# Kernel optimization log

Hardware: AMD Instinct MI355X
Metric: run time of the kernel (lower is better)

Reference implementation:

```python
import jax, jax.numpy as jnp
import numpy as np

S, B, IN, OUT = 32, 256, 1024, 1024

def setup_inputs() -> dict:
    key = jax.random.key(0)
    ks = jax.random.split(key, 7)
    return {
        "input": jax.random.normal(ks[0], (S, B, IN), dtype=jnp.float32),
        "weight_mu": jax.random.normal(ks[1], (OUT, IN), dtype=jnp.float32) * 0.1,
        "weight_rho": jax.random.normal(ks[2], (OUT, IN), dtype=jnp.float32) - 3.0,
        "bias_mu": jax.random.normal(ks[3], (OUT,), dtype=jnp.float32) * 0.1,
        "bias_rho": jax.random.normal(ks[4], (OUT,), dtype=jnp.float32) - 3.0,
        "eps_w": jax.random.normal(ks[5], (S, OUT, IN), dtype=jnp.float32),
        "eps_b": jax.random.normal(ks[6], (S, OUT), dtype=jnp.float32),
    }

def reference(input, weight_mu, weight_rho, bias_mu, bias_rho, eps_w, eps_b):
    # sigma = log(1 + exp(rho))  (softplus)
    weight_sigma = jax.nn.softplus(weight_rho)              # (out, in)
    bias_sigma = jax.nn.softplus(bias_rho)                  # (out,)
    # reparameterized samples: (S, out, in) and (S, out)
    weight = weight_mu[None, :, :] + weight_sigma[None, :, :] * eps_w
    bias = bias_mu[None, :] + bias_sigma[None, :] * eps_b
    # batch_linear: per-sample x @ W^T + b
    out = jnp.einsum('sbi,soi->sbo', input, weight) + bias[:, None, :]
    return out
```

## Files before the change

kernel.cpp:

```cpp
#include <hip/hip_runtime.h>
#include <hip/hip_bf16.h>

constexpr int kS   = 32;
constexpr int kB   = 256;
constexpr int kIN  = 1024;
constexpr int kOUT = 1024;
constexpr int BN   = 64;
constexpr int BK   = 32;
constexpr int CK   = 256;

typedef __bf16 v4bf __attribute__((ext_vector_type(4)));
typedef __bf16 v8bf __attribute__((ext_vector_type(8)));
typedef float  v4f  __attribute__((ext_vector_type(4)));

__device__ __forceinline__ float softplus_f(float x) {
    return fmaxf(x, 0.0f) + log1pf(expf(-fabsf(x)));
}
__device__ __forceinline__ unsigned int bfbits(float x) {
    __bf16 h = (__bf16)x;
    unsigned short u;
    __builtin_memcpy(&u, &h, 2);
    return (unsigned int)u;
}
__device__ __forceinline__ float asf(unsigned int u) {
    float f; __builtin_memcpy(&f, &u, 4); return f;
}

__global__ void sigma_pack(const float* __restrict__ mu, const float* __restrict__ rho,
                           uint4* __restrict__ ms) {
    int gid = blockIdx.x * blockDim.x + threadIdx.x;
    float4 m = reinterpret_cast<const float4*>(mu)[gid];
    float4 r = reinterpret_cast<const float4*>(rho)[gid];
    uint4 o;
    o.x = bfbits(m.x) | (bfbits(softplus_f(r.x)) << 16);
    o.y = bfbits(m.y) | (bfbits(softplus_f(r.y)) << 16);
    o.z = bfbits(m.z) | (bfbits(softplus_f(r.z)) << 16);
    o.w = bfbits(m.w) | (bfbits(softplus_f(r.w)) << 16);
    ms[gid] = o;
}

__global__ void xcast_kernel(const float* __restrict__ X, __bf16* __restrict__ Xb) {
    size_t i = ((size_t)blockIdx.x * blockDim.x + threadIdx.x) * 8;
    float4 a = *reinterpret_cast<const float4*>(X + i);
    float4 b = *reinterpret_cast<const float4*>(X + i + 4);
    v8bf r;
    r[0] = (__bf16)a.x; r[1] = (__bf16)a.y; r[2] = (__bf16)a.z; r[3] = (__bf16)a.w;
    r[4] = (__bf16)b.x; r[5] = (__bf16)b.y; r[6] = (__bf16)b.z; r[7] = (__bf16)b.w;
    *reinterpret_cast<v8bf*>(Xb + i) = r;
}

#define GLDS16(g, l) __builtin_amdgcn_global_load_lds(                      \
    (const __attribute__((address_space(1))) void*)(g),                     \
    (__attribute__((address_space(3))) void*)(l), 16, 0, 0)

template<bool XBF>
__global__ __launch_bounds__(256) void dv_main(
        const void* __restrict__ Xv,
        const unsigned int* __restrict__ MS,
        const float* __restrict__ Ew,
        const float* __restrict__ Bmu,
        const float* __restrict__ Brho,
        const float* __restrict__ Eb,
        float* __restrict__ O)
{
    __shared__ __attribute__((aligned(16))) __bf16 Xs[2][kB * BK];
    __shared__ __attribute__((aligned(16))) __bf16 Wc[BN * CK];

    const int tid  = threadIdx.x;
    const int bb   = blockIdx.x;
    const int xcd  = bb & 7;
    const int jj   = bb >> 3;
    const int s    = (xcd << 2) | (jj & 3);
    const int ot   = jj >> 2;
    const int o_base = ot * BN;

    const int lane = tid & 63, wv = tid >> 6;
    const int lr = lane & 15, kg = lane >> 4;

    const float*        Eg  = Ew + ((size_t)s * kOUT + o_base) * kIN;
    const unsigned int* MSg = MS + (size_t)o_base * kIN;
    const __bf16* Xb = (const __bf16*)Xv + (size_t)s * kB * kIN;
    const float*  Xg = (const float*)Xv + (size_t)s * kB * kIN;

    v4f acc[4][4] = {};

    if constexpr (XBF) {
        #pragma unroll
        for (int q = 0; q < 4; ++q) {
            int row = wv * 64 + q * 16 + (lane >> 2);
            int qg  = ((lane & 3) - (row >> 2)) & 3;
            GLDS16(Xb + (size_t)row * kIN + qg * 8, &Xs[0][(wv * 64 + q * 16) * BK]);
        }
    }

    for (int c = 0; c < 4; ++c) {
        const int ck = c * CK;

        #pragma unroll 2
        for (int j = 0; j < 8; ++j) {
            int slot = j * 256 + tid;
            int row  = slot >> 5;
            int ch   = slot & 31;
            const float*        ep = Eg  + (size_t)row * kIN + ck + ch * 8;
            const unsigned int* mp = MSg + (size_t)row * kIN + ck + ch * 8;
            float4 e0 = *reinterpret_cast<const float4*>(ep);
            float4 e1 = *reinterpret_cast<const float4*>(ep + 4);
            uint4  p0 = *reinterpret_cast<const uint4*>(mp);
            uint4  p1 = *reinterpret_cast<const uint4*>(mp + 4);
            v8bf w;
            w[0] = (__bf16)fmaf(asf(p0.x & 0xffff0000u), e0.x, asf(p0.x << 16));
            w[1] = (__bf16)fmaf(asf(p0.y & 0xffff0000u), e0.y, asf(p0.y << 16));
            w[2] = (__bf16)fmaf(asf(p0.z & 0xffff0000u), e0.z, asf(p0.z << 16));
            w[3] = (__bf16)fmaf(asf(p0.w & 0xffff0000u), e0.w, asf(p0.w << 16));
            w[4] = (__bf16)fmaf(asf(p1.x & 0xffff0000u), e1.x, asf(p1.x << 16));
            w[5] = (__bf16)fmaf(asf(p1.y & 0xffff0000u), e1.y, asf(p1.y << 16));
            w[6] = (__bf16)fmaf(asf(p1.z & 0xffff0000u), e1.z, asf(p1.z << 16));
            w[7] = (__bf16)fmaf(asf(p1.w & 0xffff0000u), e1.w, asf(p1.w << 16));
            int pos = (ch + 2 * row) & 31;
            *reinterpret_cast<v8bf*>(&Wc[row * CK + pos * 8]) = w;
        }
        __syncthreads();

        for (int t = 0; t < 8; ++t) {
            const int kt = c * 8 + t;
            const int p  = kt & 1;

            if constexpr (XBF) {
                if (kt + 1 < 32) {
                    const int kk2 = (kt + 1) * BK;
                    #pragma unroll
                    for (int q = 0; q < 4; ++q) {
                        int row = wv * 64 + q * 16 + (lane >> 2);
                        int qg  = ((lane & 3) - (row >> 2)) & 3;
                        GLDS16(Xb + (size_t)row * kIN + kk2 + qg * 8,
                               &Xs[p ^ 1][(wv * 64 + q * 16) * BK]);
                    }
                }
            } else {
                #pragma unroll
                for (int f0 = 0; f0 < 8; ++f0) {
                    int f = f0 * 256 + tid;
                    int row = f >> 3, cc = f & 7;
                    float4 v = *reinterpret_cast<const float4*>(
                        Xg + (size_t)row * kIN + kt * BK + cc * 4);
                    int q = cc >> 1, h = cc & 1;
                    int ql = (q + (row >> 2)) & 3;
                    v4bf w;
                    w[0] = (__bf16)v.x; w[1] = (__bf16)v.y;
                    w[2] = (__bf16)v.z; w[3] = (__bf16)v.w;
                    *reinterpret_cast<v4bf*>(&Xs[p][row * BK + ql * 8 + h * 4]) = w;
                }
                __syncthreads();
            }

            v8bf a[4], b[4];
            #pragma unroll
            for (int mf = 0; mf < 4; ++mf) {
                int row = wv * 64 + mf * 16 + lr;
                int ql  = (kg + (row >> 2)) & 3;
                a[mf] = *reinterpret_cast<const v8bf*>(&Xs[p][row * BK + ql * 8]);
            }
            #pragma unroll
            for (int nf = 0; nf < 4; ++nf) {
                int r   = nf * 16 + lr;
                int pos = ((t * 4 + kg) + 2 * r) & 31;
                b[nf] = *reinterpret_cast<const v8bf*>(&Wc[r * CK + pos * 8]);
            }
            #pragma unroll
            for (int mf = 0; mf < 4; ++mf) {
                #pragma unroll
                for (int nf = 0; nf < 4; ++nf)
                    acc[mf][nf] = __builtin_amdgcn_mfma_f32_16x16x32_bf16(
                        a[mf], b[nf], acc[mf][nf], 0, 0, 0);
            }
            __syncthreads();
        }
    }

    float bias[4];
    #pragma unroll
    for (int nf = 0; nf < 4; ++nf) {
        int o = o_base + nf * 16 + lr;
        bias[nf] = fmaf(softplus_f(Brho[o]), Eb[(size_t)s * kOUT + o], Bmu[o]);
    }
    #pragma unroll
    for (int mf = 0; mf < 4; ++mf) {
        #pragma unroll
        for (int rr = 0; rr < 4; ++rr) {
            int mrow = wv * 64 + mf * 16 + kg * 4 + rr;
            float* orow = O + ((size_t)s * kB + mrow) * kOUT + o_base;
            #pragma unroll
            for (int nf = 0; nf < 4; ++nf)
                orow[nf * 16 + lr] = acc[mf][nf][rr] + bias[nf];
        }
    }
}

extern "C" void kernel_launch(void* const* d_in, const int* in_sizes, int n_in,
                              void* d_out, int out_size, void* d_ws, size_t ws_size,
                              hipStream_t stream) {
    const float* input = (const float*)d_in[0];
    const float* w_mu  = (const float*)d_in[1];
    const float* w_rho = (const float*)d_in[2];
    const float* b_mu  = (const float*)d_in[3];
    const float* b_rho = (const float*)d_in[4];
    const float* eps_w = (const float*)d_in[5];
    const float* eps_b = (const float*)d_in[6];
    float* out = (float*)d_out;

    const size_t ms_bytes  = (size_t)kOUT * kIN * 4;
    const size_t xbf_bytes = (size_t)kS * kB * kIN * sizeof(__bf16);
    const bool use_xbf = ws_size >= ms_bytes + xbf_bytes;

    unsigned int* ms = (unsigned int*)d_ws;
    __bf16* xbf = (__bf16*)((char*)d_ws + ms_bytes);

    sigma_pack<<<dim3((kOUT * kIN) / (256 * 4)), 256, 0, stream>>>(w_mu, w_rho, (uint4*)ms);

    dim3 grid(kS * (kOUT / BN));
    if (use_xbf) {
        xcast_kernel<<<dim3((size_t)kS * kB * kIN / (256 * 8)), 256, 0, stream>>>(input, xbf);
        dv_main<true><<<grid, 256, 0, stream>>>(xbf, ms, eps_w, b_mu, b_rho, eps_b, out);
    } else {
        dv_main<false><<<grid, 256, 0, stream>>>(input, ms, eps_w, b_mu, b_rho, eps_b, out);
    }
}
```

Baseline: 260.1 us.

## Drop LDS staging and load MFMA operands directly from global memory

Replaces the shared-memory tiled GEMM with a register-only scheme. Each lane loads its X and weight fragments straight from global memory, and the weight is built in registers from eps and the packed mu/sigma. The output tile shrinks to 32 columns, and launch bounds are raised to allow four blocks per CU. Output stores become nontemporal, and a periodic barrier keeps the waves loosely in step. This removes LDS traffic and most barriers, but each weight element is now loaded redundantly by all four waves, and each lane's global loads are strided by rows and poorly coalesced.

```diff
diff --git a/kernel.cpp b/kernel.cpp
--- a/kernel.cpp
+++ b/kernel.cpp
@@ -5,11 +5,8 @@
 constexpr int kB   = 256;
 constexpr int kIN  = 1024;
 constexpr int kOUT = 1024;
-constexpr int BN   = 64;
-constexpr int BK   = 32;
-constexpr int CK   = 256;
+constexpr int BN   = 32;
 
-typedef __bf16 v4bf __attribute__((ext_vector_type(4)));
 typedef __bf16 v8bf __attribute__((ext_vector_type(8)));
 typedef float  v4f  __attribute__((ext_vector_type(4)));
 
@@ -49,12 +46,8 @@
     *reinterpret_cast<v8bf*>(Xb + i) = r;
 }
 
-#define GLDS16(g, l) __builtin_amdgcn_global_load_lds(                      \
-    (const __attribute__((address_space(1))) void*)(g),                     \
-    (__attribute__((address_space(3))) void*)(l), 16, 0, 0)
-
 template<bool XBF>
-__global__ __launch_bounds__(256) void dv_main(
+__global__ __launch_bounds__(256, 4) void dv_main(
         const void* __restrict__ Xv,
         const unsigned int* __restrict__ MS,
         const float* __restrict__ Ew,
@@ -63,123 +56,84 @@
         const float* __restrict__ Eb,
         float* __restrict__ O)
 {
-    __shared__ __attribute__((aligned(16))) __bf16 Xs[2][kB * BK];
-    __shared__ __attribute__((aligned(16))) __bf16 Wc[BN * CK];
-
-    const int tid  = threadIdx.x;
-    const int bb   = blockIdx.x;
-    const int xcd  = bb & 7;
-    const int jj   = bb >> 3;
-    const int s    = (xcd << 2) | (jj & 3);
-    const int ot   = jj >> 2;
-    const int o_base = ot * BN;
+    const int tid = threadIdx.x;
+    const int bb  = blockIdx.x;
+    const int xcd = bb & 7;
+    const int jj  = bb >> 3;
+    const int s   = (xcd << 2) | (jj & 3);
+    const int o_base = (jj >> 2) * BN;
 
     const int lane = tid & 63, wv = tid >> 6;
     const int lr = lane & 15, kg = lane >> 4;
 
-    const float*        Eg  = Ew + ((size_t)s * kOUT + o_base) * kIN;
-    const unsigned int* MSg = MS + (size_t)o_base * kIN;
-    const __bf16* Xb = (const __bf16*)Xv + (size_t)s * kB * kIN;
-    const float*  Xg = (const float*)Xv + (size_t)s * kB * kIN;
+    const size_t R16 = (size_t)16 * kIN;
 
-    v4f acc[4][4] = {};
+    const float*        Eg  = Ew + ((size_t)s * kOUT + o_base + lr) * kIN + kg * 8;
+    const unsigned int* MSg = MS + (size_t)(o_base + lr) * kIN + kg * 8;
+    const __bf16* Xb = (const __bf16*)Xv + ((size_t)s * kB + wv * 64 + lr) * kIN + kg * 8;
+    const float*  Xg = (const float*)Xv  + ((size_t)s * kB + wv * 64 + lr) * kIN + kg * 8;
 
-    if constexpr (XBF) {
+    v4f acc[4][2] = {};
+
+    for (int kt = 0; kt < 32; ++kt) {
+        const int k0 = kt * 32;
+
+        v8bf a[4];
+        if constexpr (XBF) {
+            #pragma unroll
+            for (int mf = 0; mf < 4; ++mf)
+                a[mf] = *reinterpret_cast<const v8bf*>(Xb + mf * R16 + k0);
+        } else {
+            #pragma unroll
+            for (int mf = 0; mf < 4; ++mf) {
+                float4 x0 = *reinterpret_cast<const float4*>(Xg + mf * R16 + k0);
+                float4 x1 = *reinterpret_cast<const float4*>(Xg + mf * R16 + k0 + 4);
+                v8bf t;
+                t[0] = (__bf16)x0.x; t[1] = (__bf16)x0.y;
+                t[2] = (__bf16)x0.z; t[3] = (__bf16)x0.w;
+                t[4] = (__bf16)x1.x; t[5] = (__bf16)x1.y;
+                t[6] = (__bf16)x1.z; t[7] = (__bf16)x1.w;
+                a[mf] = t;
+            }
+        }
+
+        float4 e0[2], e1[2]; uint4 p0[2], p1[2];
         #pragma unroll
-        for (int q = 0; q < 4; ++q) {
-            int row = wv * 64 + q * 16 + (lane >> 2);
-            int qg  = ((lane & 3) - (row >> 2)) & 3;
-            GLDS16(Xb + (size_t)row * kIN + qg * 8, &Xs[0][(wv * 64 + q * 16) * BK]);
+        for (int nf = 0; nf < 2; ++nf) {
+            const float*        ep = Eg  + nf * R16 + k0;
+            const unsigned int* mp = MSg + nf * R16 + k0;
+            e0[nf] = *reinterpret_cast<const float4*>(ep);
+            e1[nf] = *reinterpret_cast<const float4*>(ep + 4);
+            p0[nf] = *reinterpret_cast<const uint4*>(mp);
+            p1[nf] = *reinterpret_cast<const uint4*>(mp + 4);
         }
+
+        v8bf b[2];
+        #pragma unroll
+        for (int nf = 0; nf < 2; ++nf) {
+            b[nf][0] = (__bf16)fmaf(asf(p0[nf].x & 0xffff0000u), e0[nf].x, asf(p0[nf].x << 16));
+            b[nf][1] = (__bf16)fmaf(asf(p0[nf].y & 0xffff0000u), e0[nf].y, asf(p0[nf].y << 16));
+            b[nf][2] = (__bf16)fmaf(asf(p0[nf].z & 0xffff0000u), e0[nf].z, asf(p0[nf].z << 16));
+            b[nf][3] = (__bf16)fmaf(asf(p0[nf].w & 0xffff0000u), e0[nf].w, asf(p0[nf].w << 16));
+            b[nf][4] = (__bf16)fmaf(asf(p1[nf].x & 0xffff0000u), e1[nf].x, asf(p1[nf].x << 16));
+            b[nf][5] = (__bf16)fmaf(asf(p1[nf].y & 0xffff0000u), e1[nf].y, asf(p1[nf].y << 16));
+            b[nf][6] = (__bf16)fmaf(asf(p1[nf].z & 0xffff0000u), e1[nf].z, asf(p1[nf].z << 16));
+            b[nf][7] = (__bf16)fmaf(asf(p1[nf].w & 0xffff0000u), e1[nf].w, asf(p1[nf].w << 16));
+        }
+
+        #pragma unroll
+        for (int mf = 0; mf < 4; ++mf)
+            #pragma unroll
+            for (int nf = 0; nf < 2; ++nf)
+                acc[mf][nf] = __builtin_amdgcn_mfma_f32_16x16x32_bf16(
+                    a[mf], b[nf], acc[mf][nf], 0, 0, 0);
+
+        if ((kt & 7) == 7) __syncthreads();
     }
 
-    for (int c = 0; c < 4; ++c) {
-        const int ck = c * CK;
-
-        #pragma unroll 2
-        for (int j = 0; j < 8; ++j) {
-            int slot = j * 256 + tid;
-            int row  = slot >> 5;
-            int ch   = slot & 31;
-            const float*        ep = Eg  + (size_t)row * kIN + ck + ch * 8;
-            const unsigned int* mp = MSg + (size_t)row * kIN + ck + ch * 8;
-            float4 e0 = *reinterpret_cast<const float4*>(ep);
-            float4 e1 = *reinterpret_cast<const float4*>(ep + 4);
-            uint4  p0 = *reinterpret_cast<const uint4*>(mp);
-            uint4  p1 = *reinterpret_cast<const uint4*>(mp + 4);
-            v8bf w;
-            w[0] = (__bf16)fmaf(asf(p0.x & 0xffff0000u), e0.x, asf(p0.x << 16));
-            w[1] = (__bf16)fmaf(asf(p0.y & 0xffff0000u), e0.y, asf(p0.y << 16));
-            w[2] = (__bf16)fmaf(asf(p0.z & 0xffff0000u), e0.z, asf(p0.z << 16));
-            w[3] = (__bf16)fmaf(asf(p0.w & 0xffff0000u), e0.w, asf(p0.w << 16));
-            w[4] = (__bf16)fmaf(asf(p1.x & 0xffff0000u), e1.x, asf(p1.x << 16));
-            w[5] = (__bf16)fmaf(asf(p1.y & 0xffff0000u), e1.y, asf(p1.y << 16));
-            w[6] = (__bf16)fmaf(asf(p1.z & 0xffff0000u), e1.z, asf(p1.z << 16));
-            w[7] = (__bf16)fmaf(asf(p1.w & 0xffff0000u), e1.w, asf(p1.w << 16));
-            int pos = (ch + 2 * row) & 31;
-            *reinterpret_cast<v8bf*>(&Wc[row * CK + pos * 8]) = w;
-        }
-        __syncthreads();
-
-        for (int t = 0; t < 8; ++t) {
-            const int kt = c * 8 + t;
-            const int p  = kt & 1;
-
-            if constexpr (XBF) {
-                if (kt + 1 < 32) {
-                    const int kk2 = (kt + 1) * BK;
-                    #pragma unroll
-                    for (int q = 0; q < 4; ++q) {
-                        int row = wv * 64 + q * 16 + (lane >> 2);
-                        int qg  = ((lane & 3) - (row >> 2)) & 3;
-                        GLDS16(Xb + (size_t)row * kIN + kk2 + qg * 8,
-                               &Xs[p ^ 1][(wv * 64 + q * 16) * BK]);
-                    }
-                }
-            } else {
-                #pragma unroll
-                for (int f0 = 0; f0 < 8; ++f0) {
-                    int f = f0 * 256 + tid;
-                    int row = f >> 3, cc = f & 7;
-                    float4 v = *reinterpret_cast<const float4*>(
-                        Xg + (size_t)row * kIN + kt * BK + cc * 4);
-                    int q = cc >> 1, h = cc & 1;
-                    int ql = (q + (row >> 2)) & 3;
-                    v4bf w;
-                    w[0] = (__bf16)v.x; w[1] = (__bf16)v.y;
-                    w[2] = (__bf16)v.z; w[3] = (__bf16)v.w;
-                    *reinterpret_cast<v4bf*>(&Xs[p][row * BK + ql * 8 + h * 4]) = w;
-                }
-                __syncthreads();
-            }
-
-            v8bf a[4], b[4];
-            #pragma unroll
-            for (int mf = 0; mf < 4; ++mf) {
-                int row = wv * 64 + mf * 16 + lr;
-                int ql  = (kg + (row >> 2)) & 3;
-                a[mf] = *reinterpret_cast<const v8bf*>(&Xs[p][row * BK + ql * 8]);
-            }
-            #pragma unroll
-            for (int nf = 0; nf < 4; ++nf) {
-                int r   = nf * 16 + lr;
-                int pos = ((t * 4 + kg) + 2 * r) & 31;
-                b[nf] = *reinterpret_cast<const v8bf*>(&Wc[r * CK + pos * 8]);
-            }
-            #pragma unroll
-            for (int mf = 0; mf < 4; ++mf) {
-                #pragma unroll
-                for (int nf = 0; nf < 4; ++nf)
-                    acc[mf][nf] = __builtin_amdgcn_mfma_f32_16x16x32_bf16(
-                        a[mf], b[nf], acc[mf][nf], 0, 0, 0);
-            }
-            __syncthreads();
-        }
-    }
-
-    float bias[4];
+    float bias[2];
     #pragma unroll
-    for (int nf = 0; nf < 4; ++nf) {
+    for (int nf = 0; nf < 2; ++nf) {
         int o = o_base + nf * 16 + lr;
         bias[nf] = fmaf(softplus_f(Brho[o]), Eb[(size_t)s * kOUT + o], Bmu[o]);
     }
@@ -190,8 +144,9 @@
             int mrow = wv * 64 + mf * 16 + kg * 4 + rr;
             float* orow = O + ((size_t)s * kB + mrow) * kOUT + o_base;
             #pragma unroll
-            for (int nf = 0; nf < 4; ++nf)
-                orow[nf * 16 + lr] = acc[mf][nf][rr] + bias[nf];
+            for (int nf = 0; nf < 2; ++nf)
+                __builtin_nontemporal_store(acc[mf][nf][rr] + bias[nf],
+                                            orow + nf * 16 + lr);
         }
     }
 }
```

Result: slower. 372.7 us (+43.3%).
